# Performance work log

Hardware: AMD Instinct MI355X
Metric: run time of the kernel (lower is better)

The kernel has to match this reference:

```python
import jax, jax.numpy as jnp
import numpy as np

MODEL_DIM = 256
HEADS = 8
LN_EPS = 1e-5


def layer_norm(x, gamma, beta):
    mu = jnp.mean(x, axis=-1, keepdims=True)
    var = jnp.var(x, axis=-1, keepdims=True)
    return (x - mu) * jax.lax.rsqrt(var + LN_EPS) * gamma + beta


def setup_inputs() -> dict:
    key = jax.random.key(0)
    ks = jax.random.split(key, 4)
    bs, n, d, h = 16, 1024, MODEL_DIM, HEADS
    scale = 1.0 / np.sqrt(d)
    x = jax.random.normal(ks[0], (bs, n, d), dtype=jnp.float32)
    Wq = jax.random.normal(ks[1], (d * h, d), dtype=jnp.float32) * scale
    Wk = jax.random.normal(ks[2], (d * h, d), dtype=jnp.float32) * scale
    Wv = jax.random.normal(ks[3], (d, d * h), dtype=jnp.float32) * (1.0 / np.sqrt(d * h))
    gamma = jnp.ones((d,), dtype=jnp.float32)
    beta = jnp.zeros((d,), dtype=jnp.float32)
    return {"x": x, "Wq": Wq, "Wk": Wk, "Wv": Wv, "gamma": gamma, "beta": beta}


def reference(x, Wq, Wk, Wv, gamma, beta):
    bs, n, d = x.shape
    h = HEADS
    # pre-norm
    xn = layer_norm(x, gamma, beta)
    # q, k: (bs, n, h, d) -> (bs, h, n, d); torch Linear: y = x @ W.T
    q = (xn @ Wq.T).reshape(bs, n, h, d).transpose(0, 2, 1, 3)
    k = (xn @ Wk.T).reshape(bs, n, h, d).transpose(0, 2, 1, 3)
    scores = jnp.einsum('bhid,bhjd->bhij', q, k) / jnp.sqrt(jnp.float32(d))
    probs = jax.nn.softmax(scores, axis=-1)  # dropout prob = 0.0
    # shared (non-per-head) value: V = xn broadcast over heads
    context = jnp.einsum('bhij,bjd->bhid', probs, xn)
    context = context.transpose(0, 2, 1, 3).reshape(bs, n, h * d)
    out = context @ Wv.T + xn  # residual uses post-pre-norm x (as in source when pre_norm)
    return out, probs
```

## Files before the change

### kernel.cpp

```cpp
#include <hip/hip_runtime.h>
#include <stdint.h>


typedef __bf16 bh8 __attribute__((ext_vector_type(8)));
typedef float f32x4 __attribute__((ext_vector_type(4)));

#define MFMA16(a, b, c) __builtin_amdgcn_mfma_f32_16x16x32_bf16((a), (b), (c), 0, 0, 0)

__device__ __forceinline__ uint16_t f2b(float f) {
  uint32_t u = __float_as_uint(f);
  u += 0x7FFFu + ((u >> 16) & 1u);
  return (uint16_t)(u >> 16);
}
__device__ __forceinline__ uint32_t pack2(float a, float b) {
  return (uint32_t)f2b(a) | ((uint32_t)f2b(b) << 16);
}
__device__ __forceinline__ void async16(const uint16_t* g, uint16_t* l) {
  __builtin_amdgcn_global_load_lds((__attribute__((address_space(1))) const uint32_t*)g,
                                   (__attribute__((address_space(3))) uint32_t*)l, 16, 0, 0);
}

__global__ __launch_bounds__(256) void ln_kernel(
    const float* __restrict__ x, const float* __restrict__ gamma,
    const float* __restrict__ beta, float* __restrict__ xnf, uint16_t* __restrict__ xnb) {
  const int wave = threadIdx.x >> 6, lane = threadIdx.x & 63;
  const size_t row = (size_t)blockIdx.x * 4 + wave;
  const float4 v = *(const float4*)(x + row * 256 + lane * 4);
  float s = v.x + v.y + v.z + v.w;
  float ss = v.x * v.x + v.y * v.y + v.z * v.z + v.w * v.w;
#pragma unroll
  for (int d = 32; d; d >>= 1) { s += __shfl_xor(s, d); ss += __shfl_xor(ss, d); }
  const float mu = s * (1.0f / 256.0f);
  const float inv = rsqrtf(ss * (1.0f / 256.0f) - mu * mu + 1e-5f);
  const float4 g = *(const float4*)(gamma + lane * 4);
  const float4 be = *(const float4*)(beta + lane * 4);
  float4 o;
  o.x = (v.x - mu) * inv * g.x + be.x;
  o.y = (v.y - mu) * inv * g.y + be.y;
  o.z = (v.z - mu) * inv * g.z + be.z;
  o.w = (v.w - mu) * inv * g.w + be.w;
  *(float4*)(xnf + row * 256 + lane * 4) = o;
  ushort4 ob;
  ob.x = f2b(o.x); ob.y = f2b(o.y); ob.z = f2b(o.z); ob.w = f2b(o.w);
  *(ushort4*)(xnb + row * 256 + lane * 4) = ob;
}

__global__ __launch_bounds__(256) void cvt_kernel(const float* __restrict__ in,
                                                  uint16_t* __restrict__ out2, int n) {
  int i = blockIdx.x * 256 + threadIdx.x;
  if (i < n) out2[i] = f2b(in[i]);
}

__global__ __launch_bounds__(256) void transpose_xn(
    const uint16_t* __restrict__ xnb, uint16_t* __restrict__ xnT) {
  const int b = blockIdx.z, it = blockIdx.y, dt = blockIdx.x;
  __shared__ uint16_t tile[64][65];
  const int t = threadIdx.x;
  const int r = t >> 2, c0 = (t & 3) * 16;
  const uint16_t* src = xnb + ((size_t)b * 1024 + it * 64) * 256 + dt * 64;
#pragma unroll
  for (int i = 0; i < 16; ++i) tile[r][c0 + i] = src[(size_t)r * 256 + c0 + i];
  __syncthreads();
  uint16_t* dst = xnT + ((size_t)b * 256 + dt * 64) * 1024 + it * 64;
#pragma unroll
  for (int i = 0; i < 16; ++i) dst[(size_t)r * 1024 + c0 + i] = tile[c0 + i][r];
}

template <int K, int N, bool RES>
__global__ __launch_bounds__(256) void gemm_bt(
    const uint16_t* __restrict__ A, const uint16_t* __restrict__ B,
    void* __restrict__ Cv, const float* __restrict__ resid) {
  const int nwg = gridDim.x, cpx = nwg >> 3;
  const int lid = blockIdx.x;
  const int swz = (lid & 7) * cpx + (lid >> 3);
  const int m0 = (swz & 127) * 128, n0 = (swz >> 7) * 128;
  const int t = threadIdx.x;
  const int lane = t & 63, wave = t >> 6;
  const int l15 = lane & 15, quad = lane >> 4;
  const int wm = (wave >> 1) * 64, wn = (wave & 1) * 64;

  __shared__ uint16_t As[2][128 * 32];
  __shared__ uint16_t Bs[2][128 * 32];

  f32x4 acc[4][4];
#pragma unroll
  for (int mi = 0; mi < 4; ++mi)
#pragma unroll
    for (int ni = 0; ni < 4; ++ni)
#pragma unroll
      for (int r = 0; r < 4; ++r) acc[mi][ni][r] = 0.0f;

  auto stage = [&](int buf, int k0) {
#pragma unroll
    for (int j = 0; j < 2; ++j) {
      int cc = j * 256 + t;
      int row = cc >> 2, ko = (cc & 3) << 3;
      async16(A + (size_t)(m0 + row) * K + k0 + ko, &As[buf][(j * 256 + (t & ~63)) * 8]);
      async16(B + (size_t)(n0 + row) * K + k0 + ko, &Bs[buf][(j * 256 + (t & ~63)) * 8]);
    }
  };

  stage(0, 0);
  __syncthreads();
  int cur = 0;
  for (int k0 = 0; k0 < K; k0 += 32) {
    if (k0 + 32 < K) stage(cur ^ 1, k0 + 32);
    bh8 afr[4], bfr[4];
#pragma unroll
    for (int mi = 0; mi < 4; ++mi)
      afr[mi] = *(const bh8*)&As[cur][(wm + mi * 16 + l15) * 32 + quad * 8];
#pragma unroll
    for (int ni = 0; ni < 4; ++ni)
      bfr[ni] = *(const bh8*)&Bs[cur][(wn + ni * 16 + l15) * 32 + quad * 8];
#pragma unroll
    for (int mi = 0; mi < 4; ++mi)
#pragma unroll
      for (int ni = 0; ni < 4; ++ni) acc[mi][ni] = MFMA16(afr[mi], bfr[ni], acc[mi][ni]);
    __syncthreads();
    cur ^= 1;
  }
#pragma unroll
  for (int mi = 0; mi < 4; ++mi)
#pragma unroll
    for (int ni = 0; ni < 4; ++ni)
#pragma unroll
      for (int r = 0; r < 4; ++r) {
        size_t m = (size_t)(m0 + wm + mi * 16 + quad * 4 + r);
        size_t n = (size_t)(n0 + wn + ni * 16 + l15);
        if constexpr (RES) {
          ((float*)Cv)[m * N + n] = acc[mi][ni][r] + resid[m * N + n];
        } else {
          ((uint16_t*)Cv)[m * N + n] = f2b(acc[mi][ni][r]);
        }
      }
}

__global__ __launch_bounds__(256, 2) void attn_scores(
    const uint16_t* __restrict__ Qp, const uint16_t* __restrict__ Kp,
    float* __restrict__ probs) {
  const int lid = blockIdx.x;
  const int swz = (lid & 7) * 512 + (lid >> 3);
  const int z = swz >> 5, rb = swz & 31;
  const int b = z >> 3, h = z & 7;
  const int t = threadIdx.x;
  const int lane = t & 63, wave = t >> 6;
  const int l15 = lane & 15, quad = lane >> 4;
  const int m0 = rb * 32;

  const uint16_t* Qb = Qp + (size_t)b * 1024 * 2048 + (size_t)h * 256;
  const uint16_t* Kb = Kp + (size_t)b * 1024 * 2048 + (size_t)h * 256;

  __shared__ uint16_t Bs[2][512 * 32];
  __shared__ float redmax[32][4];
  __shared__ float redsum[32][4];

  f32x4 acc[2][16];
#pragma unroll
  for (int mi = 0; mi < 2; ++mi)
#pragma unroll
    for (int ni = 0; ni < 16; ++ni)
#pragma unroll
      for (int r = 0; r < 4; ++r) acc[mi][ni][r] = 0.0f;

  auto stageB = [&](int buf, int p) {
    const int k0 = (p >> 1) * 32, half = p & 1;
#pragma unroll
    for (int j = 0; j < 8; ++j) {
      int cc = j * 256 + t;
      int row = half * 512 + (cc >> 2), ko = (cc & 3) << 3;
      async16(Kb + (size_t)row * 2048 + k0 + ko, &Bs[buf][(j * 256 + (t & ~63)) * 8]);
    }
  };

  bh8 aq[2][2];
#pragma unroll
  for (int mi = 0; mi < 2; ++mi)
    aq[0][mi] = *(const bh8*)(Qb + (size_t)(m0 + mi * 16 + l15) * 2048 + quad * 8);

  stageB(0, 0);
  __syncthreads();

  int cur = 0;
#pragma unroll
  for (int p = 0; p < 16; ++p) {
    const int ks = p >> 1, half = p & 1;
    if (half == 0 && ks < 7) {
#pragma unroll
      for (int mi = 0; mi < 2; ++mi)
        aq[(ks + 1) & 1][mi] =
            *(const bh8*)(Qb + (size_t)(m0 + mi * 16 + l15) * 2048 + (ks + 1) * 32 + quad * 8);
    }
    if (p < 15) stageB(cur ^ 1, p + 1);
#pragma unroll
    for (int ni = 0; ni < 8; ++ni) {
      bh8 bf = *(const bh8*)&Bs[cur][(wave * 128 + ni * 16 + l15) * 32 + quad * 8];
      acc[0][half * 8 + ni] = MFMA16(aq[ks & 1][0], bf, acc[0][half * 8 + ni]);
      acc[1][half * 8 + ni] = MFMA16(aq[ks & 1][1], bf, acc[1][half * 8 + ni]);
    }
    __syncthreads();
    cur ^= 1;
  }

  const float sc = 0.0625f * 1.44269504f;
  float rowm[2][4];
#pragma unroll
  for (int mi = 0; mi < 2; ++mi)
#pragma unroll
    for (int r = 0; r < 4; ++r) {
      float m = acc[mi][0][r];
#pragma unroll
      for (int ni = 1; ni < 16; ++ni) m = fmaxf(m, acc[mi][ni][r]);
#pragma unroll
      for (int d = 1; d < 16; d <<= 1) m = fmaxf(m, __shfl_xor(m, d));
      rowm[mi][r] = m;
    }
  if (l15 == 0) {
#pragma unroll
    for (int mi = 0; mi < 2; ++mi)
#pragma unroll
      for (int r = 0; r < 4; ++r) redmax[mi * 16 + quad * 4 + r][wave] = rowm[mi][r];
  }
  __syncthreads();
#pragma unroll
  for (int mi = 0; mi < 2; ++mi)
#pragma unroll
    for (int r = 0; r < 4; ++r) {
      int row = mi * 16 + quad * 4 + r;
      rowm[mi][r] = fmaxf(fmaxf(redmax[row][0], redmax[row][1]),
                          fmaxf(redmax[row][2], redmax[row][3]));
    }
  float rsum[2][4];
#pragma unroll
  for (int mi = 0; mi < 2; ++mi)
#pragma unroll
    for (int r = 0; r < 4; ++r) rsum[mi][r] = 0.0f;
#pragma unroll
  for (int mi = 0; mi < 2; ++mi)
#pragma unroll
    for (int ni = 0; ni < 16; ++ni)
#pragma unroll
      for (int r = 0; r < 4; ++r) {
        float e = exp2f((acc[mi][ni][r] - rowm[mi][r]) * sc);
        acc[mi][ni][r] = e;
        rsum[mi][r] += e;
      }
#pragma unroll
  for (int mi = 0; mi < 2; ++mi)
#pragma unroll
    for (int r = 0; r < 4; ++r) {
#pragma unroll
      for (int d = 1; d < 16; d <<= 1) rsum[mi][r] += __shfl_xor(rsum[mi][r], d);
    }
  if (l15 == 0) {
#pragma unroll
    for (int mi = 0; mi < 2; ++mi)
#pragma unroll
      for (int r = 0; r < 4; ++r) redsum[mi * 16 + quad * 4 + r][wave] = rsum[mi][r];
  }
  __syncthreads();
  float rinv[2][4];
#pragma unroll
  for (int mi = 0; mi < 2; ++mi)
#pragma unroll
    for (int r = 0; r < 4; ++r) {
      int row = mi * 16 + quad * 4 + r;
      rinv[mi][r] = 1.0f / (redsum[row][0] + redsum[row][1] + redsum[row][2] + redsum[row][3]);
    }
  float* P = probs + (size_t)z * 1024 * 1024 + (size_t)m0 * 1024;
#pragma unroll
  for (int mi = 0; mi < 2; ++mi)
#pragma unroll
    for (int ni = 0; ni < 16; ++ni)
#pragma unroll
      for (int r = 0; r < 4; ++r) {
        int row = mi * 16 + quad * 4 + r;
        int col = (ni >> 3) * 512 + wave * 128 + (ni & 7) * 16 + l15;
        P[(size_t)row * 1024 + col] = acc[mi][ni][r] * rinv[mi][r];
      }
}

__global__ __launch_bounds__(256) void gemm_ctx(
    const float* __restrict__ P, const uint16_t* __restrict__ XT,
    uint16_t* __restrict__ ctx) {
  const int lid = blockIdx.x;
  const int swz = (lid & 7) * 256 + (lid >> 3);
  const int z = swz >> 4, mt = swz & 15;
  const int b = z >> 3, h = z & 7;
  const int t = threadIdx.x;
  const int lane = t & 63, wave = t >> 6;
  const int l15 = lane & 15, quad = lane >> 4;
  const int wm = (wave >> 1) * 32, wn = (wave & 1) * 128;
  const int m0 = mt * 64;
  const float* Ab = P + (size_t)z * 1024 * 1024;
  const uint16_t* Bb = XT + (size_t)b * 256 * 1024;

  __shared__ uint16_t As[2][64 * 32];
  __shared__ uint16_t Bs[2][256 * 32];

  f32x4 acc[2][8];
#pragma unroll
  for (int mi = 0; mi < 2; ++mi)
#pragma unroll
    for (int ni = 0; ni < 8; ++ni)
#pragma unroll
      for (int r = 0; r < 4; ++r) acc[mi][ni][r] = 0.0f;

  const int arow = t >> 2, aco = (t & 3) * 8;
  const float* ag = Ab + (size_t)(m0 + arow) * 1024 + aco;

  auto stageB = [&](int buf, int k0) {
#pragma unroll
    for (int j = 0; j < 4; ++j) {
      int cc = j * 256 + t;
      int row = cc >> 2, ko = (cc & 3) << 3;
      async16(Bb + (size_t)row * 1024 + k0 + ko, &Bs[buf][(j * 256 + (t & ~63)) * 8]);
    }
  };

  {
    float4 f0 = *(const float4*)(ag);
    float4 f1 = *(const float4*)(ag + 4);
    stageB(0, 0);
    uint4 pk;
    pk.x = pack2(f0.x, f0.y); pk.y = pack2(f0.z, f0.w);
    pk.z = pack2(f1.x, f1.y); pk.w = pack2(f1.z, f1.w);
    *(uint4*)&As[0][arow * 32 + aco] = pk;
  }
  __syncthreads();

  int cur = 0;
  for (int k0 = 0; k0 < 1024; k0 += 32) {
    const bool nxt = (k0 + 32) < 1024;
    float4 g0, g1;
    if (nxt) {
      g0 = *(const float4*)(ag + k0 + 32);
      g1 = *(const float4*)(ag + k0 + 36);
    }
    if (nxt) stageB(cur ^ 1, k0 + 32);
    bh8 afr[2], bfr[8];
#pragma unroll
    for (int mi = 0; mi < 2; ++mi)
      afr[mi] = *(const bh8*)&As[cur][(wm + mi * 16 + l15) * 32 + quad * 8];
#pragma unroll
    for (int ni = 0; ni < 8; ++ni)
      bfr[ni] = *(const bh8*)&Bs[cur][(wn + ni * 16 + l15) * 32 + quad * 8];
#pragma unroll
    for (int mi = 0; mi < 2; ++mi)
#pragma unroll
      for (int ni = 0; ni < 8; ++ni) acc[mi][ni] = MFMA16(afr[mi], bfr[ni], acc[mi][ni]);
    if (nxt) {
      uint4 pk;
      pk.x = pack2(g0.x, g0.y); pk.y = pack2(g0.z, g0.w);
      pk.z = pack2(g1.x, g1.y); pk.w = pack2(g1.z, g1.w);
      *(uint4*)&As[cur ^ 1][arow * 32 + aco] = pk;
    }
    __syncthreads();
    cur ^= 1;
  }
  const size_t growbase = (size_t)b * 1024 + m0 + wm;
#pragma unroll
  for (int mi = 0; mi < 2; ++mi)
#pragma unroll
    for (int ni = 0; ni < 8; ++ni)
#pragma unroll
      for (int r = 0; r < 4; ++r) {
        size_t grow = growbase + mi * 16 + quad * 4 + r;
        int col = h * 256 + wn + ni * 16 + l15;
        ctx[grow * 2048 + col] = f2b(acc[mi][ni][r]);
      }
}

extern "C" void kernel_launch(void* const* d_in, const int* in_sizes, int n_in,
                              void* d_out, int out_size, void* d_ws, size_t ws_size,
                              hipStream_t stream) {
  const float* x = (const float*)d_in[0];
  const float* Wq = (const float*)d_in[1];
  const float* Wk = (const float*)d_in[2];
  const float* Wv = (const float*)d_in[3];
  const float* gamma = (const float*)d_in[4];
  const float* beta = (const float*)d_in[5];
  float* out = (float*)d_out;
  float* probs = out + (size_t)16 * 1024 * 256;

  char* ws = (char*)d_ws;
  float* xnf = (float*)(ws + 0);
  uint16_t* xnb = (uint16_t*)(ws + 16777216);
  uint16_t* xnT = (uint16_t*)(ws + 25165824);
  uint16_t* wqb = (uint16_t*)(ws + 33554432);
  uint16_t* wkb = (uint16_t*)(ws + 34603008);
  uint16_t* wvb = (uint16_t*)(ws + 35651584);
  uint16_t* Qp = (uint16_t*)(ws + 36700160);
  uint16_t* Kp = (uint16_t*)(ws + 103809024);
  uint16_t* ctx = (uint16_t*)(ws + 170917888);

  ln_kernel<<<4096, 256, 0, stream>>>(x, gamma, beta, xnf, xnb);
  cvt_kernel<<<2048, 256, 0, stream>>>(Wq, wqb, 2048 * 256);
  cvt_kernel<<<2048, 256, 0, stream>>>(Wk, wkb, 2048 * 256);
  cvt_kernel<<<2048, 256, 0, stream>>>(Wv, wvb, 256 * 2048);
  transpose_xn<<<dim3(4, 16, 16), 256, 0, stream>>>(xnb, xnT);
  gemm_bt<256, 2048, false><<<2048, 256, 0, stream>>>(xnb, wqb, (void*)Qp, nullptr);
  gemm_bt<256, 2048, false><<<2048, 256, 0, stream>>>(xnb, wkb, (void*)Kp, nullptr);
  attn_scores<<<4096, 256, 0, stream>>>(Qp, Kp, probs);
  gemm_ctx<<<2048, 256, 0, stream>>>(probs, xnT, ctx);
  gemm_bt<2048, 256, true><<<256, 256, 0, stream>>>(ctx, wvb, (void*)out, xnf);
}
```

Baseline: 1.121 ms.

## Fuse probs-times-V GEMM into attention scores kernel via LDS-staged probabilities

Merges the separate context GEMM into the attention-scores kernel. The normalized probabilities are written to global memory with nontemporal stores and also kept as bf16 in a padded LDS tile, then multiplied against the transposed normalized input in two halves. This removes the full re-read of the fp32 probs tensor, about 512MB, and its conversion in a second kernel. It also adds s_setprio around the MFMA loops and reuses LDS through a union, which raises shared-memory pressure and may cost occupancy.

```diff
diff --git a/kernel.cpp b/kernel.cpp
--- a/kernel.cpp
+++ b/kernel.cpp
@@ -112,10 +112,12 @@
 #pragma unroll
     for (int ni = 0; ni < 4; ++ni)
       bfr[ni] = *(const bh8*)&Bs[cur][(wn + ni * 16 + l15) * 32 + quad * 8];
+    __builtin_amdgcn_s_setprio(1);
 #pragma unroll
     for (int mi = 0; mi < 4; ++mi)
 #pragma unroll
       for (int ni = 0; ni < 4; ++ni) acc[mi][ni] = MFMA16(afr[mi], bfr[ni], acc[mi][ni]);
+    __builtin_amdgcn_s_setprio(0);
     __syncthreads();
     cur ^= 1;
   }
@@ -135,9 +137,10 @@
       }
 }
 
-__global__ __launch_bounds__(256, 2) void attn_scores(
+__global__ __launch_bounds__(256, 2) void attn_fused(
     const uint16_t* __restrict__ Qp, const uint16_t* __restrict__ Kp,
-    float* __restrict__ probs) {
+    const uint16_t* __restrict__ XT, float* __restrict__ probs,
+    uint16_t* __restrict__ ctx) {
   const int lid = blockIdx.x;
   const int swz = (lid & 7) * 512 + (lid >> 3);
   const int z = swz >> 5, rb = swz & 31;
@@ -149,8 +152,14 @@
 
   const uint16_t* Qb = Qp + (size_t)b * 1024 * 2048 + (size_t)h * 256;
   const uint16_t* Kb = Kp + (size_t)b * 1024 * 2048 + (size_t)h * 256;
-
-  __shared__ uint16_t Bs[2][512 * 32];
+  const uint16_t* Xb = XT + (size_t)b * 256 * 1024;
+
+  constexpr int PP = 520;
+  union U {
+    uint16_t qkBs[2][512 * 32];
+    struct { uint16_t P[32 * PP]; uint16_t Bx[2][256 * 32]; } pv;
+  };
+  __shared__ U u;
   __shared__ float redmax[32][4];
   __shared__ float redsum[32][4];
 
@@ -168,7 +177,7 @@
     for (int j = 0; j < 8; ++j) {
       int cc = j * 256 + t;
       int row = half * 512 + (cc >> 2), ko = (cc & 3) << 3;
-      async16(Kb + (size_t)row * 2048 + k0 + ko, &Bs[buf][(j * 256 + (t & ~63)) * 8]);
+      async16(Kb + (size_t)row * 2048 + k0 + ko, &u.qkBs[buf][(j * 256 + (t & ~63)) * 8]);
     }
   };
 
@@ -191,12 +200,14 @@
             *(const bh8*)(Qb + (size_t)(m0 + mi * 16 + l15) * 2048 + (ks + 1) * 32 + quad * 8);
     }
     if (p < 15) stageB(cur ^ 1, p + 1);
+    __builtin_amdgcn_s_setprio(1);
 #pragma unroll
     for (int ni = 0; ni < 8; ++ni) {
-      bh8 bf = *(const bh8*)&Bs[cur][(wave * 128 + ni * 16 + l15) * 32 + quad * 8];
+      bh8 bf = *(const bh8*)&u.qkBs[cur][(wave * 128 + ni * 16 + l15) * 32 + quad * 8];
       acc[0][half * 8 + ni] = MFMA16(aq[ks & 1][0], bf, acc[0][half * 8 + ni]);
       acc[1][half * 8 + ni] = MFMA16(aq[ks & 1][1], bf, acc[1][half * 8 + ni]);
     }
+    __builtin_amdgcn_s_setprio(0);
     __syncthreads();
     cur ^= 1;
   }
@@ -266,107 +277,100 @@
       int row = mi * 16 + quad * 4 + r;
       rinv[mi][r] = 1.0f / (redsum[row][0] + redsum[row][1] + redsum[row][2] + redsum[row][3]);
     }
-  float* P = probs + (size_t)z * 1024 * 1024 + (size_t)m0 * 1024;
-#pragma unroll
-  for (int mi = 0; mi < 2; ++mi)
-#pragma unroll
-    for (int ni = 0; ni < 16; ++ni)
-#pragma unroll
-      for (int r = 0; r < 4; ++r) {
-        int row = mi * 16 + quad * 4 + r;
-        int col = (ni >> 3) * 512 + wave * 128 + (ni & 7) * 16 + l15;
-        P[(size_t)row * 1024 + col] = acc[mi][ni][r] * rinv[mi][r];
-      }
-}
-
-__global__ __launch_bounds__(256) void gemm_ctx(
-    const float* __restrict__ P, const uint16_t* __restrict__ XT,
-    uint16_t* __restrict__ ctx) {
-  const int lid = blockIdx.x;
-  const int swz = (lid & 7) * 256 + (lid >> 3);
-  const int z = swz >> 4, mt = swz & 15;
-  const int b = z >> 3, h = z & 7;
-  const int t = threadIdx.x;
-  const int lane = t & 63, wave = t >> 6;
-  const int l15 = lane & 15, quad = lane >> 4;
-  const int wm = (wave >> 1) * 32, wn = (wave & 1) * 128;
-  const int m0 = mt * 64;
-  const float* Ab = P + (size_t)z * 1024 * 1024;
-  const uint16_t* Bb = XT + (size_t)b * 256 * 1024;
-
-  __shared__ uint16_t As[2][64 * 32];
-  __shared__ uint16_t Bs[2][256 * 32];
-
-  f32x4 acc[2][8];
-#pragma unroll
-  for (int mi = 0; mi < 2; ++mi)
-#pragma unroll
-    for (int ni = 0; ni < 8; ++ni)
-#pragma unroll
-      for (int r = 0; r < 4; ++r) acc[mi][ni][r] = 0.0f;
-
-  const int arow = t >> 2, aco = (t & 3) * 8;
-  const float* ag = Ab + (size_t)(m0 + arow) * 1024 + aco;
-
-  auto stageB = [&](int buf, int k0) {
+
+  float* Pg = probs + (size_t)z * 1024 * 1024 + (size_t)m0 * 1024;
+
+  auto stageX = [&](int buf, int k0) {
 #pragma unroll
     for (int j = 0; j < 4; ++j) {
       int cc = j * 256 + t;
       int row = cc >> 2, ko = (cc & 3) << 3;
-      async16(Bb + (size_t)row * 1024 + k0 + ko, &Bs[buf][(j * 256 + (t & ~63)) * 8]);
+      async16(Xb + (size_t)row * 1024 + k0 + ko, &u.pv.Bx[buf][(j * 256 + (t & ~63)) * 8]);
     }
   };
 
-  {
-    float4 f0 = *(const float4*)(ag);
-    float4 f1 = *(const float4*)(ag + 4);
-    stageB(0, 0);
-    uint4 pk;
-    pk.x = pack2(f0.x, f0.y); pk.y = pack2(f0.z, f0.w);
-    pk.z = pack2(f1.x, f1.y); pk.w = pack2(f1.z, f1.w);
-    *(uint4*)&As[0][arow * 32 + aco] = pk;
-  }
-  __syncthreads();
-
-  int cur = 0;
-  for (int k0 = 0; k0 < 1024; k0 += 32) {
-    const bool nxt = (k0 + 32) < 1024;
-    float4 g0, g1;
-    if (nxt) {
-      g0 = *(const float4*)(ag + k0 + 32);
-      g1 = *(const float4*)(ag + k0 + 36);
-    }
-    if (nxt) stageB(cur ^ 1, k0 + 32);
-    bh8 afr[2], bfr[8];
-#pragma unroll
-    for (int mi = 0; mi < 2; ++mi)
-      afr[mi] = *(const bh8*)&As[cur][(wm + mi * 16 + l15) * 32 + quad * 8];
+  f32x4 acc2[2][4];
+#pragma unroll
+  for (int mi = 0; mi < 2; ++mi)
+#pragma unroll
+    for (int ni = 0; ni < 4; ++ni)
+#pragma unroll
+      for (int r = 0; r < 4; ++r) acc2[mi][ni][r] = 0.0f;
+
+#pragma unroll
+  for (int mi = 0; mi < 2; ++mi)
 #pragma unroll
     for (int ni = 0; ni < 8; ++ni)
-      bfr[ni] = *(const bh8*)&Bs[cur][(wn + ni * 16 + l15) * 32 + quad * 8];
-#pragma unroll
-    for (int mi = 0; mi < 2; ++mi)
-#pragma unroll
-      for (int ni = 0; ni < 8; ++ni) acc[mi][ni] = MFMA16(afr[mi], bfr[ni], acc[mi][ni]);
-    if (nxt) {
-      uint4 pk;
-      pk.x = pack2(g0.x, g0.y); pk.y = pack2(g0.z, g0.w);
-      pk.z = pack2(g1.x, g1.y); pk.w = pack2(g1.z, g1.w);
-      *(uint4*)&As[cur ^ 1][arow * 32 + aco] = pk;
-    }
+#pragma unroll
+      for (int r = 0; r < 4; ++r) {
+        int row = mi * 16 + quad * 4 + r;
+        int colh = wave * 128 + ni * 16 + l15;
+        float v = acc[mi][ni][r] * rinv[mi][r];
+        __builtin_nontemporal_store(v, &Pg[(size_t)row * 1024 + colh]);
+        u.pv.P[row * PP + colh] = f2b(v);
+      }
+  stageX(0, 0);
+  __syncthreads();
+
+  cur = 0;
+#pragma unroll
+  for (int ks = 0; ks < 16; ++ks) {
+    stageX(cur ^ 1, ks * 32 + 32);
+    bh8 pa0 = *(const bh8*)&u.pv.P[l15 * PP + ks * 32 + quad * 8];
+    bh8 pa1 = *(const bh8*)&u.pv.P[(16 + l15) * PP + ks * 32 + quad * 8];
+    __builtin_amdgcn_s_setprio(1);
+#pragma unroll
+    for (int ni = 0; ni < 4; ++ni) {
+      bh8 bx = *(const bh8*)&u.pv.Bx[cur][(wave * 64 + ni * 16 + l15) * 32 + quad * 8];
+      acc2[0][ni] = MFMA16(pa0, bx, acc2[0][ni]);
+      acc2[1][ni] = MFMA16(pa1, bx, acc2[1][ni]);
+    }
+    __builtin_amdgcn_s_setprio(0);
     __syncthreads();
     cur ^= 1;
   }
-  const size_t growbase = (size_t)b * 1024 + m0 + wm;
+
 #pragma unroll
   for (int mi = 0; mi < 2; ++mi)
 #pragma unroll
     for (int ni = 0; ni < 8; ++ni)
+#pragma unroll
+      for (int r = 0; r < 4; ++r) {
+        int row = mi * 16 + quad * 4 + r;
+        int colh = wave * 128 + ni * 16 + l15;
+        float v = acc[mi][8 + ni][r] * rinv[mi][r];
+        __builtin_nontemporal_store(v, &Pg[(size_t)row * 1024 + 512 + colh]);
+        u.pv.P[row * PP + colh] = f2b(v);
+      }
+  __syncthreads();
+
+#pragma unroll
+  for (int ks = 0; ks < 16; ++ks) {
+    if (ks < 15) stageX(cur ^ 1, 512 + ks * 32 + 32);
+    bh8 pa0 = *(const bh8*)&u.pv.P[l15 * PP + ks * 32 + quad * 8];
+    bh8 pa1 = *(const bh8*)&u.pv.P[(16 + l15) * PP + ks * 32 + quad * 8];
+    __builtin_amdgcn_s_setprio(1);
+#pragma unroll
+    for (int ni = 0; ni < 4; ++ni) {
+      bh8 bx = *(const bh8*)&u.pv.Bx[cur][(wave * 64 + ni * 16 + l15) * 32 + quad * 8];
+      acc2[0][ni] = MFMA16(pa0, bx, acc2[0][ni]);
+      acc2[1][ni] = MFMA16(pa1, bx, acc2[1][ni]);
+    }
+    __builtin_amdgcn_s_setprio(0);
+    __syncthreads();
+    cur ^= 1;
+  }
+
+  const size_t growbase = (size_t)b * 1024 + m0;
+#pragma unroll
+  for (int mi = 0; mi < 2; ++mi)
+#pragma unroll
+    for (int ni = 0; ni < 4; ++ni)
 #pragma unroll
       for (int r = 0; r < 4; ++r) {
         size_t grow = growbase + mi * 16 + quad * 4 + r;
-        int col = h * 256 + wn + ni * 16 + l15;
-        ctx[grow * 2048 + col] = f2b(acc[mi][ni][r]);
+        int col = h * 256 + wave * 64 + ni * 16 + l15;
+        ctx[grow * 2048 + col] = f2b(acc2[mi][ni][r]);
       }
 }
 
@@ -400,7 +404,6 @@
   transpose_xn<<<dim3(4, 16, 16), 256, 0, stream>>>(xnb, xnT);
   gemm_bt<256, 2048, false><<<2048, 256, 0, stream>>>(xnb, wqb, (void*)Qp, nullptr);
   gemm_bt<256, 2048, false><<<2048, 256, 0, stream>>>(xnb, wkb, (void*)Kp, nullptr);
-  attn_scores<<<4096, 256, 0, stream>>>(Qp, Kp, probs);
-  gemm_ctx<<<2048, 256, 0, stream>>>(probs, xnT, ctx);
+  attn_fused<<<4096, 256, 0, stream>>>(Qp, Kp, xnT, probs, ctx);
   gemm_bt<2048, 256, true><<<256, 256, 0, stream>>>(ctx, wvb, (void*)out, xnf);
 }
```

Result: faster. 1.009 ms (-10.0%).
